# Kernel optimization log

Measured on AMD Instinct MI355X. Metric: run time of the kernel, lower is better.

Reference implementation:

```python
import jax, jax.numpy as jnp
import numpy as np

HIDDEN = 1024
HEADS = 16
BATCH = 2
SEQ = 2048
# dropout_p = 0.1 but module evaluated in eval mode (training=False) -> identity


def setup_inputs() -> dict:
    key = jax.random.key(0)
    k1, k2, k3 = jax.random.split(key, 3)
    x = jax.random.normal(k1, (BATCH, SEQ, HIDDEN), dtype=jnp.float32)
    # unit-scaling Linear: weight ~ N(0,1) (reset_parameters uses nn.init.normal_)
    w_qkv = jax.random.normal(k2, (3 * HIDDEN, HIDDEN), dtype=jnp.float32)
    w_o = jax.random.normal(k3, (HIDDEN, HIDDEN), dtype=jnp.float32)
    return {"x": x, "w_qkv": w_qkv, "w_o": w_o}


def reference(x, w_qkv, w_o):
    b, s, hid = x.shape
    heads = HEADS
    d = hid // heads
    # unit-scaled linear (constraint='to_output_scale'): y = x @ W.T * fan_in**-0.5
    qkv = (x @ w_qkv.T) * (hid ** -0.5)            # [b, s, 3*hid]
    # einops 'b s (z h d) -> z b h s d'
    qkv = qkv.reshape(b, s, 3, heads, d)
    q = jnp.transpose(qkv[:, :, 0], (0, 2, 1, 3))   # [b, h, s, d]
    k = jnp.transpose(qkv[:, :, 1], (0, 2, 1, 3))
    v = jnp.transpose(qkv[:, :, 2], (0, 2, 1, 3))
    # unit-scaled matmul: scale = inner_dim**-0.5
    scores = jnp.einsum('bhqd,bhkd->bhqk', q, k) * (d ** -0.5)  # [b, h, s, s]
    # unit-scaled softmax: output_scale = n / sqrt(n - 1)
    attn = jax.nn.softmax(scores, axis=-1) * (s / np.sqrt(s - 1.0))
    # dropout inactive (eval mode)
    out = jnp.einsum('bhqk,bhkd->bhqd', attn, v) * (s ** -0.5)  # inner dim = s
    out = jnp.transpose(out, (0, 2, 1, 3)).reshape(b, s, hid)   # 'b h s d -> b s (h d)'
    return (out @ w_o.T) * (hid ** -0.5)
```

## Files before the change

### kernel.cpp

```cpp
#include <hip/hip_runtime.h>

typedef unsigned short u16;
typedef _Float16 f16x8 __attribute__((ext_vector_type(8)));
typedef _Float16 f16x4 __attribute__((ext_vector_type(4)));
typedef float f32x4 __attribute__((ext_vector_type(4)));
typedef unsigned short u16x4 __attribute__((ext_vector_type(4)));

#define HID 1024
#define SEQ 2048
#define NH 16
#define DH 64

__device__ __forceinline__ u16 f2h(float f) {
  return __builtin_bit_cast(u16, (_Float16)f);
}
__device__ __forceinline__ f32x4 mfma_h(f16x8 a, f16x8 b, f32x4 c) {
  return __builtin_amdgcn_mfma_f32_16x16x32_f16(a, b, c, 0, 0, 0);
}
__device__ __forceinline__ f32x4 mfma_h16(f16x4 a, f16x4 b, f32x4 c) {
  return __builtin_amdgcn_mfma_f32_16x16x16f16(a, b, c, 0, 0, 0);
}
__device__ __forceinline__ float fexp2(float x) {
#if __has_builtin(__builtin_amdgcn_exp2f)
  return __builtin_amdgcn_exp2f(x);
#else
  return __expf(0.69314718f * x);
#endif
}
__device__ __forceinline__ void g2l16(const u16* g, u16* l) {
  __builtin_amdgcn_global_load_lds(
      (const __attribute__((address_space(1))) unsigned int*)g,
      (__attribute__((address_space(3))) unsigned int*)l, 16, 0, 0);
}

#define NX4 ((4096 * 1024) / 4)
#define NQ4 ((3072 * 1024) / 4)
#define NO4 ((1024 * 1024) / 4)
__global__ __launch_bounds__(256) void prep_kernel(
    const float* __restrict__ x, const float* __restrict__ wq,
    const float* __restrict__ wo,
    u16* __restrict__ x16, u16* __restrict__ wq16, u16* __restrict__ wo16) {
  int i = blockIdx.x * 256 + threadIdx.x;
  const float4 v = (i < NX4) ? ((const float4*)x)[i]
                 : (i < NX4 + NQ4) ? ((const float4*)wq)[i - NX4]
                 : ((const float4*)wo)[i - NX4 - NQ4];
  u16* dst = (i < NX4) ? &x16[(size_t)i * 4]
           : (i < NX4 + NQ4) ? &wq16[(size_t)(i - NX4) * 4]
           : &wo16[(size_t)(i - NX4 - NQ4) * 4];
  u16x4 o;
  o[0] = f2h(v.x); o[1] = f2h(v.y); o[2] = f2h(v.z); o[3] = f2h(v.w);
  *(u16x4*)dst = o;
}

__global__ __launch_bounds__(256, 3) void gemm_qkv(
    const u16* __restrict__ a16, const u16* __restrict__ b16,
    u16* __restrict__ qf, u16* __restrict__ kf, u16* __restrict__ vtf) {
  __shared__ __align__(16) u16 la[128 * 32], lb[128 * 32];
  const int t = threadIdx.x;
  const int lane = t & 63, w = t >> 6;
  const int wr = w >> 1, wc = w & 1;
  const int lr = lane & 15, lg = lane >> 4;
  const int br = blockIdx.x, bc = blockIdx.y;
  const f32x4 fzero = {0.f, 0.f, 0.f, 0.f};
  f32x4 acc[4][4];
#pragma unroll
  for (int i = 0; i < 4; ++i)
#pragma unroll
    for (int j = 0; j < 4; ++j) acc[i][j] = fzero;
  const int srow = t >> 2, scol = (t & 3) << 3;
  const u16* ga = a16 + (size_t)(br * 128 + srow) * HID + scol;
  const u16* gb = b16 + (size_t)(bc * 128 + srow) * HID + scol;
  const int lo16 = t * 8;
  for (int kk = 0; kk < HID; kk += 32) {
    g2l16(ga + kk, &la[lo16]);
    g2l16(ga + kk + (size_t)64 * HID, &la[lo16 + 2048]);
    g2l16(gb + kk, &lb[lo16]);
    g2l16(gb + kk + (size_t)64 * HID, &lb[lo16 + 2048]);
    __syncthreads();
    f16x8 ah[4], bh[4];
#pragma unroll
    for (int i = 0; i < 4; ++i)
      ah[i] = *(const f16x8*)&la[(wr * 64 + i * 16 + lr) * 32 + lg * 8];
#pragma unroll
    for (int j = 0; j < 4; ++j)
      bh[j] = *(const f16x8*)&lb[(wc * 64 + j * 16 + lr) * 32 + lg * 8];
#pragma unroll
    for (int i = 0; i < 4; ++i)
#pragma unroll
      for (int j = 0; j < 4; ++j) acc[i][j] = mfma_h(ah[i], bh[j], acc[i][j]);
    __syncthreads();
  }
  const int m0 = br * 128 + wr * 64, n0 = bc * 128 + wc * 64;
#pragma unroll
  for (int i = 0; i < 4; ++i)
#pragma unroll
    for (int j = 0; j < 4; ++j)
#pragma unroll
      for (int r = 0; r < 4; ++r) {
        int row = m0 + i * 16 + lg * 4 + r;
        int col = n0 + j * 16 + lr;
        float val = acc[i][j][r] * 0.03125f;
        int b = row >> 11, s = row & 2047;
        int z = col >> 10, hh = (col >> 6) & 15, d = col & 63;
        int bhid = b * NH + hh;
        if (z == 0) {
          qf[((size_t)bhid * SEQ + s) * DH + d] = f2h(val * 0.18033688f);
        } else if (z == 1) {
          kf[((size_t)bhid * SEQ + s) * DH + d] = f2h(val);
        } else {
          int kv = s & 63;
          int ct = kv >> 4, lgv = (kv >> 2) & 3, rv = kv & 3;
          int kvp = ((ct >> 1) << 5) | (lgv << 3) | ((ct & 1) << 2) | rv;
          int s2 = (s & ~63) | kvp;
          vtf[((size_t)bhid * DH + d) * SEQ + s2] = f2h(val);
        }
      }
}

__global__ __launch_bounds__(256, 2) void gemm_proj(
    const u16* __restrict__ a16, const u16* __restrict__ b16,
    float* __restrict__ out) {
  __shared__ __align__(16) u16 la[128 * 32];
  __shared__ __align__(16) u16 lb[64 * 32];
  const int t = threadIdx.x;
  const int lane = t & 63, w = t >> 6;
  const int wr = w >> 1, wc = w & 1;
  const int lr = lane & 15, lg = lane >> 4;
  const int br = blockIdx.x, bc = blockIdx.y;
  const f32x4 fzero = {0.f, 0.f, 0.f, 0.f};
  f32x4 acc[4][2];
#pragma unroll
  for (int i = 0; i < 4; ++i)
#pragma unroll
    for (int j = 0; j < 2; ++j) acc[i][j] = fzero;
  const int srow = t >> 2, scol = (t & 3) << 3;
  const u16* ga = a16 + (size_t)(br * 128 + srow) * HID + scol;
  const u16* gb = b16 + (size_t)(bc * 64 + srow) * HID + scol;
  const int lo16 = t * 8;
  for (int kk = 0; kk < HID; kk += 32) {
    g2l16(ga + kk, &la[lo16]);
    g2l16(ga + kk + (size_t)64 * HID, &la[lo16 + 2048]);
    g2l16(gb + kk, &lb[lo16]);
    __syncthreads();
    f16x8 ah[4], bh[2];
#pragma unroll
    for (int i = 0; i < 4; ++i)
      ah[i] = *(const f16x8*)&la[(wr * 64 + i * 16 + lr) * 32 + lg * 8];
#pragma unroll
    for (int j = 0; j < 2; ++j)
      bh[j] = *(const f16x8*)&lb[(wc * 32 + j * 16 + lr) * 32 + lg * 8];
#pragma unroll
    for (int i = 0; i < 4; ++i)
#pragma unroll
      for (int j = 0; j < 2; ++j)
        acc[i][j] = mfma_h(ah[i], bh[j], acc[i][j]);
    __syncthreads();
  }
  const int m0 = br * 128 + wr * 64, n0 = bc * 64 + wc * 32;
#pragma unroll
  for (int i = 0; i < 4; ++i)
#pragma unroll
    for (int j = 0; j < 2; ++j)
#pragma unroll
      for (int r = 0; r < 4; ++r) {
        int row = m0 + i * 16 + lg * 4 + r;
        int col = n0 + j * 16 + lr;
        out[(size_t)row * HID + col] = acc[i][j][r] * 0.03125f;
      }
}

__global__ __launch_bounds__(256, 2) void attn_kernel(
    const u16* __restrict__ qf, const u16* __restrict__ kf,
    const u16* __restrict__ vtf, u16* __restrict__ o16) {
  __shared__ __align__(16) u16 lk[2][64 * 64];
  __shared__ __align__(16) u16 lv[2][64 * 64];
  const int t = threadIdx.x;
  const int lane = t & 63, w = t >> 6;
  const int lr = lane & 15, lg = lane >> 4;
  const int bh = blockIdx.x, qt = blockIdx.y;
  const size_t base_qk = (size_t)bh * SEQ * DH;
  const size_t base_vt = (size_t)bh * DH * SEQ;

  f16x8 qfr[2][2];
#pragma unroll
  for (int rt = 0; rt < 2; ++rt)
#pragma unroll
    for (int ks = 0; ks < 2; ++ks)
      qfr[rt][ks] = *(const f16x8*)&qf[base_qk +
          (size_t)(qt * 128 + w * 32 + rt * 16 + lr) * DH + ks * 32 + lg * 8];

  f16x4 bI;
#pragma unroll
  for (int j = 0; j < 4; ++j) bI[j] = (_Float16)((lr == lg * 4 + j) ? 1.0f : 0.0f);

  const f32x4 fzero = {0.f, 0.f, 0.f, 0.f};
  f32x4 acc_o[2][4];
  float l_i[2][4];
#pragma unroll
  for (int rt = 0; rt < 2; ++rt)
#pragma unroll
    for (int r = 0; r < 4; ++r) l_i[rt][r] = 0.f;
#pragma unroll
  for (int rt = 0; rt < 2; ++rt)
#pragma unroll
    for (int ct = 0; ct < 4; ++ct) acc_o[rt][ct] = fzero;

  const int srow = t >> 3;
  const int scol = ((t & 7) ^ (srow & 7)) << 3;
  const int lo16 = t * 8;

  const u16* gk0 = kf + base_qk + (size_t)srow * DH + scol;
  const u16* gv0 = vtf + base_vt + (size_t)srow * SEQ + scol;

#define STAGE(buf, j)                                             \
  {                                                               \
    const u16* gk = gk0 + (size_t)(j) * 64 * DH;                  \
    g2l16(gk, &lk[buf][lo16]);                                    \
    g2l16(gk + 32 * DH, &lk[buf][lo16 + 2048]);                   \
    const u16* gv = gv0 + (j) * 64;                               \
    g2l16(gv, &lv[buf][lo16]);                                    \
    g2l16(gv + (size_t)32 * SEQ, &lv[buf][lo16 + 2048]);          \
  }

  STAGE(0, 0)

  for (int j = 0; j < SEQ / 64; ++j) {
    const int cur = j & 1;
    __syncthreads();

    f32x4 sa[2][4];
#pragma unroll
    for (int rt = 0; rt < 2; ++rt)
#pragma unroll
      for (int ct = 0; ct < 4; ++ct) sa[rt][ct] = fzero;
#pragma unroll
    for (int ks = 0; ks < 2; ++ks)
#pragma unroll
      for (int ct = 0; ct < 4; ++ct) {
        int row = ct * 16 + lr;
        f16x8 kfr = *(const f16x8*)&lk[cur][row * 64 + (((ks * 4 + lg) ^ (row & 7)) << 3)];
#pragma unroll
        for (int rt = 0; rt < 2; ++rt) sa[rt][ct] = mfma_h(qfr[rt][ks], kfr, sa[rt][ct]);
      }

    if (j + 1 < SEQ / 64) STAGE(cur ^ 1, j + 1)

    f16x8 pfr[2][2];
#pragma unroll
    for (int rt = 0; rt < 2; ++rt) {
      f32x4 tr[4];
#pragma unroll
      for (int ct = 0; ct < 4; ++ct) {
        f16x4 a4;
#pragma unroll
        for (int r = 0; r < 4; ++r) {
          float p = fexp2(sa[rt][ct][r]);
          l_i[rt][r] += p;
          a4[r] = (_Float16)p;
        }
        tr[ct] = mfma_h16(a4, bI, fzero);
      }
#pragma unroll
      for (int ks = 0; ks < 2; ++ks) {
        f16x8 pf;
#pragma unroll
        for (int j2 = 0; j2 < 8; ++j2)
          pf[j2] = (_Float16)tr[ks * 2 + (j2 >> 2)][j2 & 3];
        pfr[rt][ks] = pf;
      }
    }

#pragma unroll
    for (int ks = 0; ks < 2; ++ks)
#pragma unroll
      for (int ct = 0; ct < 4; ++ct) {
        int vrow = ct * 16 + lr;
        f16x8 vfr = *(const f16x8*)&lv[cur][vrow * 64 + (((ks * 4 + lg) ^ (vrow & 7)) << 3)];
#pragma unroll
        for (int rt = 0; rt < 2; ++rt) acc_o[rt][ct] = mfma_h(pfr[rt][ks], vfr, acc_o[rt][ct]);
      }
  }

#pragma unroll
  for (int rt = 0; rt < 2; ++rt)
#pragma unroll
    for (int r = 0; r < 4; ++r) {
      float l = l_i[rt][r];
      l += __shfl_xor(l, 1, 16);
      l += __shfl_xor(l, 2, 16);
      l += __shfl_xor(l, 4, 16);
      l += __shfl_xor(l, 8, 16);
      l_i[rt][r] = l;
    }

  const int b = bh >> 4, hh = bh & 15;
  const float fact = 1.00024426f;
#pragma unroll
  for (int rt = 0; rt < 2; ++rt)
#pragma unroll
    for (int r = 0; r < 4; ++r) {
      float inv = fact / l_i[rt][r];
      int s = qt * 128 + w * 32 + rt * 16 + lg * 4 + r;
#pragma unroll
      for (int ct = 0; ct < 4; ++ct) {
        int d = ct * 16 + lr;
        float val = acc_o[rt][ct][r] * inv;
        o16[((size_t)(b * SEQ + s)) * HID + hh * DH + d] = f2h(val);
      }
    }
}

extern "C" void kernel_launch(void* const* d_in, const int* in_sizes, int n_in,
                              void* d_out, int out_size, void* d_ws, size_t ws_size,
                              hipStream_t stream) {
  const float* x = (const float*)d_in[0];
  const float* w_qkv = (const float*)d_in[1];
  const float* w_o = (const float*)d_in[2];
  u16* ws = (u16*)d_ws;
  const size_t XS = (size_t)4096 * 1024;
  const size_t WQ = (size_t)3072 * 1024;
  const size_t WO = (size_t)1024 * 1024;
  u16* x16  = ws;           u16* wq16 = x16 + XS;
  u16* wo16 = wq16 + WQ;
  u16* q_f  = wo16 + WO;    u16* k_f  = q_f + XS;
  u16* vt_f = k_f + XS;     u16* o16  = vt_f + XS;

  prep_kernel<<<(NX4 + NQ4 + NO4) / 256, 256, 0, stream>>>(
      x, w_qkv, w_o, x16, wq16, wo16);
  gemm_qkv<<<dim3(32, 24), 256, 0, stream>>>(x16, wq16, q_f, k_f, vt_f);
  attn_kernel<<<dim3(32, 16), 256, 0, stream>>>(q_f, k_f, vt_f, o16);
  gemm_proj<<<dim3(32, 16), 256, 0, stream>>>(o16, wo16, (float*)d_out);
}
```

Measured before the change: 178.4 us.

## Deepen GEMM K-tile to 64, packed f16 conversions and MFMA priority in attention

```diff
diff --git a/kernel.cpp b/kernel.cpp
--- a/kernel.cpp
+++ b/kernel.cpp
@@ -3,6 +3,7 @@
 typedef unsigned short u16;
 typedef _Float16 f16x8 __attribute__((ext_vector_type(8)));
 typedef _Float16 f16x4 __attribute__((ext_vector_type(4)));
+typedef _Float16 f16x2 __attribute__((ext_vector_type(2)));
 typedef float f32x4 __attribute__((ext_vector_type(4)));
 typedef unsigned short u16x4 __attribute__((ext_vector_type(4)));
 
@@ -26,6 +27,9 @@
 #else
   return __expf(0.69314718f * x);
 #endif
+}
+__device__ __forceinline__ f16x2 pkrtz(float a, float b) {
+  return __builtin_bit_cast(f16x2, __builtin_amdgcn_cvt_pkrtz(a, b));
 }
 __device__ __forceinline__ void g2l16(const u16* g, u16* l) {
   __builtin_amdgcn_global_load_lds(
@@ -55,7 +59,7 @@
 __global__ __launch_bounds__(256, 3) void gemm_qkv(
     const u16* __restrict__ a16, const u16* __restrict__ b16,
     u16* __restrict__ qf, u16* __restrict__ kf, u16* __restrict__ vtf) {
-  __shared__ __align__(16) u16 la[128 * 32], lb[128 * 32];
+  __shared__ __align__(16) u16 la[128 * 64], lb[128 * 64];
   const int t = threadIdx.x;
   const int lane = t & 63, w = t >> 6;
   const int wr = w >> 1, wc = w & 1;
@@ -67,27 +71,32 @@
   for (int i = 0; i < 4; ++i)
 #pragma unroll
     for (int j = 0; j < 4; ++j) acc[i][j] = fzero;
-  const int srow = t >> 2, scol = (t & 3) << 3;
+  const int srow = t >> 3, scol = (t & 7) << 3;
   const u16* ga = a16 + (size_t)(br * 128 + srow) * HID + scol;
   const u16* gb = b16 + (size_t)(bc * 128 + srow) * HID + scol;
   const int lo16 = t * 8;
-  for (int kk = 0; kk < HID; kk += 32) {
-    g2l16(ga + kk, &la[lo16]);
-    g2l16(ga + kk + (size_t)64 * HID, &la[lo16 + 2048]);
-    g2l16(gb + kk, &lb[lo16]);
-    g2l16(gb + kk + (size_t)64 * HID, &lb[lo16 + 2048]);
-    __syncthreads();
-    f16x8 ah[4], bh[4];
-#pragma unroll
-    for (int i = 0; i < 4; ++i)
-      ah[i] = *(const f16x8*)&la[(wr * 64 + i * 16 + lr) * 32 + lg * 8];
-#pragma unroll
-    for (int j = 0; j < 4; ++j)
-      bh[j] = *(const f16x8*)&lb[(wc * 64 + j * 16 + lr) * 32 + lg * 8];
-#pragma unroll
-    for (int i = 0; i < 4; ++i)
-#pragma unroll
-      for (int j = 0; j < 4; ++j) acc[i][j] = mfma_h(ah[i], bh[j], acc[i][j]);
+  for (int kk = 0; kk < HID; kk += 64) {
+#pragma unroll
+    for (int r = 0; r < 4; ++r)
+      g2l16(ga + kk + (size_t)(r * 32) * HID, &la[lo16 + r * 2048]);
+#pragma unroll
+    for (int r = 0; r < 4; ++r)
+      g2l16(gb + kk + (size_t)(r * 32) * HID, &lb[lo16 + r * 2048]);
+    __syncthreads();
+#pragma unroll
+    for (int ks = 0; ks < 2; ++ks) {
+      f16x8 ah[4], bh[4];
+#pragma unroll
+      for (int i = 0; i < 4; ++i)
+        ah[i] = *(const f16x8*)&la[(wr * 64 + i * 16 + lr) * 64 + ks * 32 + lg * 8];
+#pragma unroll
+      for (int j = 0; j < 4; ++j)
+        bh[j] = *(const f16x8*)&lb[(wc * 64 + j * 16 + lr) * 64 + ks * 32 + lg * 8];
+#pragma unroll
+      for (int i = 0; i < 4; ++i)
+#pragma unroll
+        for (int j = 0; j < 4; ++j) acc[i][j] = mfma_h(ah[i], bh[j], acc[i][j]);
+    }
     __syncthreads();
   }
   const int m0 = br * 128 + wr * 64, n0 = bc * 128 + wc * 64;
@@ -120,8 +129,8 @@
 __global__ __launch_bounds__(256, 2) void gemm_proj(
     const u16* __restrict__ a16, const u16* __restrict__ b16,
     float* __restrict__ out) {
-  __shared__ __align__(16) u16 la[128 * 32];
-  __shared__ __align__(16) u16 lb[64 * 32];
+  __shared__ __align__(16) u16 la[128 * 64];
+  __shared__ __align__(16) u16 lb[64 * 64];
   const int t = threadIdx.x;
   const int lane = t & 63, w = t >> 6;
   const int wr = w >> 1, wc = w & 1;
@@ -133,27 +142,33 @@
   for (int i = 0; i < 4; ++i)
 #pragma unroll
     for (int j = 0; j < 2; ++j) acc[i][j] = fzero;
-  const int srow = t >> 2, scol = (t & 3) << 3;
+  const int srow = t >> 3, scol = (t & 7) << 3;
   const u16* ga = a16 + (size_t)(br * 128 + srow) * HID + scol;
   const u16* gb = b16 + (size_t)(bc * 64 + srow) * HID + scol;
   const int lo16 = t * 8;
-  for (int kk = 0; kk < HID; kk += 32) {
-    g2l16(ga + kk, &la[lo16]);
-    g2l16(ga + kk + (size_t)64 * HID, &la[lo16 + 2048]);
-    g2l16(gb + kk, &lb[lo16]);
-    __syncthreads();
-    f16x8 ah[4], bh[2];
-#pragma unroll
-    for (int i = 0; i < 4; ++i)
-      ah[i] = *(const f16x8*)&la[(wr * 64 + i * 16 + lr) * 32 + lg * 8];
-#pragma unroll
-    for (int j = 0; j < 2; ++j)
-      bh[j] = *(const f16x8*)&lb[(wc * 32 + j * 16 + lr) * 32 + lg * 8];
-#pragma unroll
-    for (int i = 0; i < 4; ++i)
+  for (int kk = 0; kk < HID; kk += 64) {
+#pragma unroll
+    for (int r = 0; r < 4; ++r)
+      g2l16(ga + kk + (size_t)(r * 32) * HID, &la[lo16 + r * 2048]);
+#pragma unroll
+    for (int r = 0; r < 2; ++r)
+      g2l16(gb + kk + (size_t)(r * 32) * HID, &lb[lo16 + r * 2048]);
+    __syncthreads();
+#pragma unroll
+    for (int ks = 0; ks < 2; ++ks) {
+      f16x8 ah[4], bh[2];
+#pragma unroll
+      for (int i = 0; i < 4; ++i)
+        ah[i] = *(const f16x8*)&la[(wr * 64 + i * 16 + lr) * 64 + ks * 32 + lg * 8];
 #pragma unroll
       for (int j = 0; j < 2; ++j)
-        acc[i][j] = mfma_h(ah[i], bh[j], acc[i][j]);
+        bh[j] = *(const f16x8*)&lb[(wc * 32 + j * 16 + lr) * 64 + ks * 32 + lg * 8];
+#pragma unroll
+      for (int i = 0; i < 4; ++i)
+#pragma unroll
+        for (int j = 0; j < 2; ++j)
+          acc[i][j] = mfma_h(ah[i], bh[j], acc[i][j]);
+    }
     __syncthreads();
   }
   const int m0 = br * 128 + wr * 64, n0 = bc * 64 + wc * 32;
@@ -233,6 +248,7 @@
     for (int rt = 0; rt < 2; ++rt)
 #pragma unroll
       for (int ct = 0; ct < 4; ++ct) sa[rt][ct] = fzero;
+    __builtin_amdgcn_s_setprio(1);
 #pragma unroll
     for (int ks = 0; ks < 2; ++ks)
 #pragma unroll
@@ -242,6 +258,7 @@
 #pragma unroll
         for (int rt = 0; rt < 2; ++rt) sa[rt][ct] = mfma_h(qfr[rt][ks], kfr, sa[rt][ct]);
       }
+    __builtin_amdgcn_s_setprio(0);
 
     if (j + 1 < SEQ / 64) STAGE(cur ^ 1, j + 1)
 
@@ -251,25 +268,29 @@
       f32x4 tr[4];
 #pragma unroll
       for (int ct = 0; ct < 4; ++ct) {
-        f16x4 a4;
-#pragma unroll
-        for (int r = 0; r < 4; ++r) {
-          float p = fexp2(sa[rt][ct][r]);
-          l_i[rt][r] += p;
-          a4[r] = (_Float16)p;
-        }
-        tr[ct] = mfma_h16(a4, bI, fzero);
+        float p0 = fexp2(sa[rt][ct][0]);
+        float p1 = fexp2(sa[rt][ct][1]);
+        float p2 = fexp2(sa[rt][ct][2]);
+        float p3 = fexp2(sa[rt][ct][3]);
+        l_i[rt][0] += p0; l_i[rt][1] += p1;
+        l_i[rt][2] += p2; l_i[rt][3] += p3;
+        union { f16x2 h2[2]; f16x4 h4; } ua;
+        ua.h2[0] = pkrtz(p0, p1);
+        ua.h2[1] = pkrtz(p2, p3);
+        tr[ct] = mfma_h16(ua.h4, bI, fzero);
       }
 #pragma unroll
       for (int ks = 0; ks < 2; ++ks) {
-        f16x8 pf;
-#pragma unroll
-        for (int j2 = 0; j2 < 8; ++j2)
-          pf[j2] = (_Float16)tr[ks * 2 + (j2 >> 2)][j2 & 3];
-        pfr[rt][ks] = pf;
-      }
-    }
-
+        union { f16x2 h2[4]; f16x8 h8; } up;
+        up.h2[0] = pkrtz(tr[ks * 2][0], tr[ks * 2][1]);
+        up.h2[1] = pkrtz(tr[ks * 2][2], tr[ks * 2][3]);
+        up.h2[2] = pkrtz(tr[ks * 2 + 1][0], tr[ks * 2 + 1][1]);
+        up.h2[3] = pkrtz(tr[ks * 2 + 1][2], tr[ks * 2 + 1][3]);
+        pfr[rt][ks] = up.h8;
+      }
+    }
+
+    __builtin_amdgcn_s_setprio(1);
 #pragma unroll
     for (int ks = 0; ks < 2; ++ks)
 #pragma unroll
@@ -279,6 +300,7 @@
 #pragma unroll
         for (int rt = 0; rt < 2; ++rt) acc_o[rt][ct] = mfma_h(pfr[rt][ks], vfr, acc_o[rt][ct]);
       }
+    __builtin_amdgcn_s_setprio(0);
   }
 
 #pragma unroll
```

Result: no change. 181.8 us (+1.9%).
